# Optimization experiments

Measured on AMD Instinct MI355X. Metric: run time of the kernel, lower is better.

The kernel has to match this reference:

```python
import jax, jax.numpy as jnp
from jax import lax
import numpy as np

B, S, I = 128, 1024, 512
H = 512  # must equal I (W_hr/W_hi are applied to h)


def setup_inputs() -> dict:
    key = jax.random.key(0)
    ks = jax.random.split(key, 10)
    s = 1.0 / np.sqrt(H)
    return {
        "inputs": jax.random.normal(ks[0], (B, S, I), jnp.float32),
        "W_ih": jax.random.normal(ks[1], (I, H), jnp.float32) * s,
        "W_hh": jax.random.normal(ks[2], (H, H), jnp.float32) * s,
        "W_ir": jax.random.normal(ks[3], (I, 1), jnp.float32) * s,
        "W_hr": jax.random.normal(ks[4], (I, 1), jnp.float32) * s,
        "W_ii": jax.random.normal(ks[5], (I, 1), jnp.float32) * s,
        "W_hi": jax.random.normal(ks[6], (I, 1), jnp.float32) * s,
        "bias_h": jax.random.normal(ks[7], (H,), jnp.float32) * s,
        "bias_r": jax.random.normal(ks[8], (1,), jnp.float32) * s,
        "bias_i": jax.random.normal(ks[9], (1,), jnp.float32) * s,
    }


def reference(inputs, W_ih, W_hh, W_ir, W_hr, W_ii, W_hi, bias_h, bias_r, bias_i):
    b = inputs.shape[0]
    h_dim = W_hh.shape[0]
    # Precompute all input projections in one batched GEMM each.
    xh = inputs @ W_ih + bias_h            # (B,S,H)
    xr = inputs @ W_ir + bias_r            # (B,S,1)
    xi = inputs @ W_ii + bias_i            # (B,S,1)

    def step(h, xs):
        xh_t, xr_t, xi_t = xs              # (B,H), (B,1), (B,1)
        z = jax.nn.sigmoid(xr_t + h @ W_hr)        # update gate (B,1)
        r = jax.nn.sigmoid(xi_t + h @ W_hi)        # reset gate  (B,1)
        n = jnp.tanh(xh_t + (r * h) @ W_hh)        # candidate   (B,H)
        h_new = z * h + (1.0 - z) * n
        return h_new, h_new

    xs = (jnp.swapaxes(xh, 0, 1), jnp.swapaxes(xr, 0, 1), jnp.swapaxes(xi, 0, 1))
    h0 = jnp.zeros((b, h_dim), inputs.dtype)
    h_last, hs = lax.scan(step, h0, xs)    # hs: (S,B,H)
    return jnp.swapaxes(hs, 0, 1), h_last
```

## Files before the change

### kernel.cpp

```cpp
#include <hip/hip_runtime.h>
#include <hip/hip_bf16.h>

#define Bd 128
#define Sd 1024
#define Id 512
#define Hd 512

#define NG 8
#define NC 8
#define BB 16
#define JW 64

typedef __attribute__((ext_vector_type(8))) short short8;
typedef __attribute__((ext_vector_type(4))) float f32x4;

__device__ __forceinline__ unsigned int bf16_rn_bits(float x){
  unsigned int bx = __float_as_uint(x);
  return (bx + 0x7FFFu + ((bx >> 16) & 1u)) >> 16;
}

__global__ __launch_bounds__(256) void k_xh(const float* __restrict__ X,
                                            const float* __restrict__ W,
                                            const float* __restrict__ bias,
                                            float* __restrict__ out)
{
  const int bidm = blockIdx.x >> 2;
  const int bidn = blockIdx.x & 3;
  const int t  = threadIdx.x;
  const int tx = t & 15, ty = t >> 4;

  __shared__ __align__(16) float At[16][132];
  __shared__ __align__(16) float Bt[16][132];

  float acc[8][8];
  #pragma unroll
  for (int i = 0; i < 8; ++i)
    #pragma unroll
    for (int j = 0; j < 8; ++j) acc[i][j] = 0.f;

  const float* Xb = X + (size_t)bidm * 128 * Id;
  const float* Wb = W + bidn * 128;

  for (int k0 = 0; k0 < Id; k0 += 16) {
    #pragma unroll
    for (int f = t; f < 512; f += 256) {
      int m = f >> 2, c = (f & 3) * 4;
      float4 v = *(const float4*)(Xb + (size_t)m * Id + k0 + c);
      At[c + 0][m] = v.x; At[c + 1][m] = v.y; At[c + 2][m] = v.z; At[c + 3][m] = v.w;
    }
    #pragma unroll
    for (int f = t; f < 512; f += 256) {
      int kr = f >> 5, nc = (f & 31) * 4;
      *(float4*)&Bt[kr][nc] = *(const float4*)(Wb + (size_t)(k0 + kr) * Hd + nc);
    }
    __syncthreads();
    #pragma unroll
    for (int k = 0; k < 16; ++k) {
      float a[8], b[8];
      *(float4*)(a)     = *(float4*)&At[k][ty * 4];
      *(float4*)(a + 4) = *(float4*)&At[k][64 + ty * 4];
      *(float4*)(b)     = *(float4*)&Bt[k][tx * 4];
      *(float4*)(b + 4) = *(float4*)&Bt[k][64 + tx * 4];
      #pragma unroll
      for (int i = 0; i < 8; ++i)
        #pragma unroll
        for (int j = 0; j < 8; ++j)
          acc[i][j] = fmaf(a[i], b[j], acc[i][j]);
    }
    __syncthreads();
  }

  float bj[8];
  *(float4*)(bj)     = *(const float4*)(bias + bidn * 128 + tx * 4);
  *(float4*)(bj + 4) = *(const float4*)(bias + bidn * 128 + 64 + tx * 4);
  size_t obase = (size_t)bidm * 128 * Hd + bidn * 128;
  #pragma unroll
  for (int i = 0; i < 8; ++i) {
    int m = (i < 4) ? (ty * 4 + i) : (64 + ty * 4 + i - 4);
    float o[8];
    #pragma unroll
    for (int j = 0; j < 8; ++j) o[j] = acc[i][j] + bj[j];
    *(float4*)(out + obase + (size_t)m * Hd + tx * 4)      = *(float4*)(o);
    *(float4*)(out + obase + (size_t)m * Hd + 64 + tx * 4) = *(float4*)(o + 4);
  }
}

__global__ __launch_bounds__(256) void k_xri(const float* __restrict__ X,
                                             const float* __restrict__ Wir,
                                             const float* __restrict__ Wii,
                                             const float* __restrict__ br,
                                             const float* __restrict__ bi,
                                             float* __restrict__ xrp,
                                             float* __restrict__ xip)
{
  const int lane = threadIdx.x & 63;
  const int wv   = threadIdx.x >> 6;
  const size_t row = (size_t)blockIdx.x * 4 + wv;
  const float* xp = X + row * Id + lane * 8;
  float4 x0 = *(const float4*)(xp);
  float4 x1 = *(const float4*)(xp + 4);
  float4 r0 = *(const float4*)(Wir + lane * 8);
  float4 r1 = *(const float4*)(Wir + lane * 8 + 4);
  float4 i0 = *(const float4*)(Wii + lane * 8);
  float4 i1 = *(const float4*)(Wii + lane * 8 + 4);
  float sr = x0.x*r0.x + x0.y*r0.y + x0.z*r0.z + x0.w*r0.w
           + x1.x*r1.x + x1.y*r1.y + x1.z*r1.z + x1.w*r1.w;
  float si = x0.x*i0.x + x0.y*i0.y + x0.z*i0.z + x0.w*i0.w
           + x1.x*i1.x + x1.y*i1.y + x1.z*i1.z + x1.w*i1.w;
  #pragma unroll
  for (int o = 32; o; o >>= 1) { sr += __shfl_xor(sr, o, 64); si += __shfl_xor(si, o, 64); }
  if (lane == 0) { xrp[row] = sr + br[0]; xip[row] = si + bi[0]; }
}

__global__ __launch_bounds__(256, 1) void k_scan(
    const float* __restrict__ xr, const float* __restrict__ xi,
    const float* __restrict__ Whh, const float* __restrict__ Whr,
    const float* __restrict__ Whi,
    float* __restrict__ hs, float* __restrict__ hlast,
    float* __restrict__ xbuf, int* __restrict__ flags)
{
  const int bid  = blockIdx.x;
  const int g    = bid & 7;
  const int c    = bid >> 3;
  const int tid  = threadIdx.x;
  const int lane = tid & 63;
  const int wv   = tid >> 6;
  const int bBase = g * BB;
  const int jBase = c * JW;

  __shared__ __align__(16) float hsm[BB][Hd];
  __shared__ __align__(16) unsigned short hhi[BB * Hd];
  __shared__ __align__(16) unsigned short hlo[BB * Hd];
  __shared__ __align__(16) float whr_s[Hd];
  __shared__ __align__(16) float whi_s[Hd];
  __shared__ float zbuf[BB], rbuf[BB];

  for (int i = tid; i < Hd; i += 256) { whr_s[i] = Whr[i]; whi_s[i] = Whi[i]; }
  for (int i = tid; i < BB * Hd / 4; i += 256) ((float4*)hsm)[i] = make_float4(0, 0, 0, 0);
  for (int i = tid; i < BB * Hd / 2; i += 256) { ((unsigned int*)hhi)[i] = 0u; ((unsigned int*)hlo)[i] = 0u; }

  const int n16 = lane & 15, kq = lane >> 4;
  const int jglob = jBase + wv * 16 + n16;
  short8 wfh[16], wfl[16];
  #pragma unroll
  for (int kt = 0; kt < 16; ++kt) {
    short8 ph, pl;
    #pragma unroll
    for (int i = 0; i < 8; ++i) {
      int k = kt * 32 + kq * 8 + i;
      float x = Whh[(size_t)k * Hd + jglob];
      unsigned int hb = bf16_rn_bits(x);
      float hf = __uint_as_float(hb << 16);
      unsigned int lb = bf16_rn_bits(x - hf);
      ph[i] = (short)hb;
      pl[i] = (short)lb;
    }
    wfh[kt] = ph; wfl[kt] = pl;
  }
  __syncthreads();

  const int myflag = g * NC + c;

  for (int t = 0; t < Sd; ++t) {
    {
      int b = tid >> 4, l16 = tid & 15;
      float sr = 0.f, si = 0.f;
      #pragma unroll
      for (int kk = 0; kk < 8; ++kk) {
        float4 hv  = *(float4*)&hsm[b][kk * 64 + l16 * 4];
        float4 wr  = *(float4*)&whr_s[kk * 64 + l16 * 4];
        float4 wi2 = *(float4*)&whi_s[kk * 64 + l16 * 4];
        sr += hv.x*wr.x  + hv.y*wr.y  + hv.z*wr.z  + hv.w*wr.w;
        si += hv.x*wi2.x + hv.y*wi2.y + hv.z*wi2.z + hv.w*wi2.w;
      }
      #pragma unroll
      for (int o = 8; o; o >>= 1) { sr += __shfl_xor(sr, o, 64); si += __shfl_xor(si, o, 64); }
      if (l16 == 0) {
        size_t bg = bBase + b;
        zbuf[b] = 1.f / (1.f + __expf(-(xr[bg * Sd + t] + sr)));
        rbuf[b] = 1.f / (1.f + __expf(-(xi[bg * Sd + t] + si)));
      }
    }
    __syncthreads();

    float xhv[4];
    #pragma unroll
    for (int r2 = 0; r2 < 4; ++r2) {
      int m = (lane >> 4) * 4 + r2;
      xhv[r2] = hs[((size_t)(bBase + m) * Sd + t) * Hd + jglob];
    }

    f32x4 a0 = {0,0,0,0}, a1 = {0,0,0,0}, a2 = {0,0,0,0};
    {
      const int abase = (lane & 15) * 1024 + (lane >> 4) * 16;
      const int sw = (lane & 7) << 4;
      #pragma unroll
      for (int kt = 0; kt < 16; ++kt) {
        int off = (abase + kt * 64) ^ sw;
        short8 ah = *(short8*)((char*)hhi + off);
        short8 al = *(short8*)((char*)hlo + off);
        a0 = __builtin_amdgcn_mfma_f32_16x16x32_bf16(ah, wfh[kt], a0, 0, 0, 0);
        a1 = __builtin_amdgcn_mfma_f32_16x16x32_bf16(ah, wfl[kt], a1, 0, 0, 0);
        a2 = __builtin_amdgcn_mfma_f32_16x16x32_bf16(al, wfh[kt], a2, 0, 0, 0);
      }
    }

    {
      int par = (t + 1) & 1;
      float* xslot = xbuf + ((size_t)g * 2 + par) * BB * Hd;
      #pragma unroll
      for (int r2 = 0; r2 < 4; ++r2) {
        int m = (lane >> 4) * 4 + r2;
        float v  = a0[r2] + a1[r2] + a2[r2];
        float rr = rbuf[m], zz = zbuf[m];
        float xv = xhv[r2] + rr * v;
        float n  = 1.f - 2.f / (__expf(2.f * xv) + 1.f);
        float hnew = zz * hsm[m][jglob] + (1.f - zz) * n;
        hs[((size_t)(bBase + m) * Sd + t) * Hd + jglob] = hnew;
        if (t == Sd - 1) hlast[(size_t)(bBase + m) * Hd + jglob] = hnew;
        xslot[(size_t)m * Hd + jglob] = hnew;
      }
    }
    __syncthreads();
    if (tid == 0) {
      __threadfence();
      __hip_atomic_store(&flags[myflag], t + 1, __ATOMIC_RELAXED, __HIP_MEMORY_SCOPE_AGENT);
    }
    if (tid < NC) {
      while (__hip_atomic_load(&flags[g * NC + tid], __ATOMIC_RELAXED, __HIP_MEMORY_SCOPE_AGENT) <= t)
        __builtin_amdgcn_s_sleep(1);
    }
    __syncthreads();
    __threadfence();

    {
      int par = (t + 1) & 1;
      const float* xslot = xbuf + ((size_t)g * 2 + par) * BB * Hd;
      #pragma unroll
      for (int i = 0; i < 8; ++i) {
        int fid = i * 256 + tid;
        float4 hv = *(const float4*)(xslot + (size_t)fid * 4);
        int b = fid >> 7, kc = fid & 127;
        *(float4*)&hsm[b][kc * 4] = hv;
        float hf4[4] = {hv.x, hv.y, hv.z, hv.w};
        unsigned long long ph = 0ull, pl = 0ull;
        #pragma unroll
        for (int j2 = 0; j2 < 4; ++j2) {
          unsigned int hb = bf16_rn_bits(hf4[j2]);
          float hff = __uint_as_float(hb << 16);
          unsigned int lb = bf16_rn_bits(hf4[j2] - hff);
          ph |= (unsigned long long)(hb & 0xFFFFu) << (16 * j2);
          pl |= (unsigned long long)(lb & 0xFFFFu) << (16 * j2);
        }
        int off = (b * 1024 + kc * 8) ^ ((b & 7) << 4);
        *(unsigned long long*)((char*)hhi + off) = ph;
        *(unsigned long long*)((char*)hlo + off) = pl;
      }
    }
    __syncthreads();
  }
}

extern "C" void kernel_launch(void* const* d_in, const int* in_sizes, int n_in,
                              void* d_out, int out_size, void* d_ws, size_t ws_size,
                              hipStream_t stream)
{
  const float* X    = (const float*)d_in[0];
  const float* Wih  = (const float*)d_in[1];
  const float* Whh  = (const float*)d_in[2];
  const float* Wir  = (const float*)d_in[3];
  const float* Whr  = (const float*)d_in[4];
  const float* Wii  = (const float*)d_in[5];
  const float* Whi  = (const float*)d_in[6];
  const float* bh   = (const float*)d_in[7];
  const float* br   = (const float*)d_in[8];
  const float* bi   = (const float*)d_in[9];
  (void)in_sizes; (void)n_in; (void)out_size;

  float* out   = (float*)d_out;
  float* hlast = out + (size_t)Bd * Sd * Hd;

  char*  ws    = (char*)d_ws;
  float* xr    = (float*)(ws);
  float* xi    = (float*)(ws + (size_t)Bd * Sd * 4);
  float* xbuf  = (float*)(ws + (size_t)Bd * Sd * 8);
  int*   flags = (int*)  (ws + (size_t)Bd * Sd * 8 + (size_t)NG * 2 * BB * Hd * 4);
  (void)ws_size;

  hipMemsetAsync(flags, 0, NG * NC * sizeof(int), stream);
  k_xh  <<<dim3(4096),            dim3(256), 0, stream>>>(X, Wih, bh, out);
  k_xri <<<dim3(Bd * Sd / 4),     dim3(256), 0, stream>>>(X, Wir, Wii, br, bi, xr, xi);
  k_scan<<<dim3(NG * NC),         dim3(256), 0, stream>>>(xr, xi, Whh, Whr, Whi, out, hlast, xbuf, flags);
}
```

Before: 10.70 ms.

## Use one 1024-thread block per batch group and MFMA split-bf16 for input GEMM

The scan kernel drops the 64-block grid and its global flag-based inter-block barrier. It uses 8 blocks of 1024 threads, each holding all of W_hh in registers as split bf16 fragments, so every timestep synchronises only inside a block. The input-projection GEMM moves from fp32 FMA to bf16 hi/lo split MFMA, and the next step's xh/xr/xi values are prefetched. The trade-off is that only 8 CUs run the serial recurrence, with heavy register pressure per thread (64 short8 weight fragments), against removing the cross-block global-memory handshake on every step.

```diff
diff --git a/kernel.cpp b/kernel.cpp
--- a/kernel.cpp
+++ b/kernel.cpp
@@ -7,9 +7,7 @@
 #define Hd 512
 
 #define NG 8
-#define NC 8
 #define BB 16
-#define JW 64
 
 typedef __attribute__((ext_vector_type(8))) short short8;
 typedef __attribute__((ext_vector_type(4))) float f32x4;
@@ -17,6 +15,12 @@
 __device__ __forceinline__ unsigned int bf16_rn_bits(float x){
   unsigned int bx = __float_as_uint(x);
   return (bx + 0x7FFFu + ((bx >> 16) & 1u)) >> 16;
+}
+__device__ __forceinline__ void bf16_split(float x, unsigned short& hi, unsigned short& lo){
+  unsigned int hb = bf16_rn_bits(x);
+  float hf = __uint_as_float(hb << 16);
+  hi = (unsigned short)hb;
+  lo = (unsigned short)bf16_rn_bits(x - hf);
 }
 
 __global__ __launch_bounds__(256) void k_xh(const float* __restrict__ X,
@@ -26,63 +30,98 @@
 {
   const int bidm = blockIdx.x >> 2;
   const int bidn = blockIdx.x & 3;
-  const int t  = threadIdx.x;
-  const int tx = t & 15, ty = t >> 4;
-
-  __shared__ __align__(16) float At[16][132];
-  __shared__ __align__(16) float Bt[16][132];
-
-  float acc[8][8];
-  #pragma unroll
-  for (int i = 0; i < 8; ++i)
-    #pragma unroll
-    for (int j = 0; j < 8; ++j) acc[i][j] = 0.f;
+  const int tid  = threadIdx.x;
+  const int lane = tid & 63;
+  const int wv   = tid >> 6;
+  const int wr   = wv >> 1, wc = wv & 1;
+  const int n16  = lane & 15, kq = lane >> 4;
+
+  __shared__ __align__(16) unsigned short Ah[128 * 64];
+  __shared__ __align__(16) unsigned short Al[128 * 64];
+  __shared__ __align__(16) unsigned short Bh[128 * 64];
+  __shared__ __align__(16) unsigned short Bl[128 * 64];
+
+  f32x4 acc[4][4];
+  #pragma unroll
+  for (int i = 0; i < 4; ++i)
+    #pragma unroll
+    for (int j = 0; j < 4; ++j) acc[i][j] = (f32x4){0.f, 0.f, 0.f, 0.f};
 
   const float* Xb = X + (size_t)bidm * 128 * Id;
   const float* Wb = W + bidn * 128;
 
-  for (int k0 = 0; k0 < Id; k0 += 16) {
-    #pragma unroll
-    for (int f = t; f < 512; f += 256) {
-      int m = f >> 2, c = (f & 3) * 4;
-      float4 v = *(const float4*)(Xb + (size_t)m * Id + k0 + c);
-      At[c + 0][m] = v.x; At[c + 1][m] = v.y; At[c + 2][m] = v.z; At[c + 3][m] = v.w;
-    }
-    #pragma unroll
-    for (int f = t; f < 512; f += 256) {
-      int kr = f >> 5, nc = (f & 31) * 4;
-      *(float4*)&Bt[kr][nc] = *(const float4*)(Wb + (size_t)(k0 + kr) * Hd + nc);
-    }
-    __syncthreads();
-    #pragma unroll
-    for (int k = 0; k < 16; ++k) {
-      float a[8], b[8];
-      *(float4*)(a)     = *(float4*)&At[k][ty * 4];
-      *(float4*)(a + 4) = *(float4*)&At[k][64 + ty * 4];
-      *(float4*)(b)     = *(float4*)&Bt[k][tx * 4];
-      *(float4*)(b + 4) = *(float4*)&Bt[k][64 + tx * 4];
-      #pragma unroll
-      for (int i = 0; i < 8; ++i)
+  for (int k0 = 0; k0 < Id; k0 += 64) {
+    #pragma unroll
+    for (int f = 0; f < 8; ++f) {
+      int idx = f * 256 + tid;
+      int m = idx >> 4, kc = (idx & 15) * 4;
+      float4 v = *(const float4*)(Xb + (size_t)m * Id + k0 + kc);
+      unsigned short h0,l0,h1,l1,h2,l2,h3,l3;
+      bf16_split(v.x,h0,l0); bf16_split(v.y,h1,l1);
+      bf16_split(v.z,h2,l2); bf16_split(v.w,h3,l3);
+      unsigned long long ph = (unsigned long long)h0 | ((unsigned long long)h1<<16)
+                            | ((unsigned long long)h2<<32) | ((unsigned long long)h3<<48);
+      unsigned long long pl = (unsigned long long)l0 | ((unsigned long long)l1<<16)
+                            | ((unsigned long long)l2<<32) | ((unsigned long long)l3<<48);
+      int off = (m * 128 + kc * 2) ^ ((m & 7) << 4);
+      *(unsigned long long*)((char*)Ah + off) = ph;
+      *(unsigned long long*)((char*)Al + off) = pl;
+    }
+    #pragma unroll
+    for (int f = 0; f < 8; ++f) {
+      int idx = f * 256 + tid;
+      int kr = idx >> 5, nc = (idx & 31) * 4;
+      float4 v = *(const float4*)(Wb + (size_t)(k0 + kr) * Hd + nc);
+      float vv[4] = {v.x, v.y, v.z, v.w};
+      #pragma unroll
+      for (int q = 0; q < 4; ++q) {
+        unsigned short h, l; bf16_split(vv[q], h, l);
+        int n = nc + q;
+        int off = (n * 128 + kr * 2) ^ ((n & 7) << 4);
+        *(unsigned short*)((char*)Bh + off) = h;
+        *(unsigned short*)((char*)Bl + off) = l;
+      }
+    }
+    __syncthreads();
+    #pragma unroll
+    for (int kt = 0; kt < 2; ++kt) {
+      short8 amh[4], aml[4];
+      #pragma unroll
+      for (int mt = 0; mt < 4; ++mt) {
+        int m = wr * 64 + mt * 16 + n16;
+        int off = (m * 128 + kt * 64 + kq * 16) ^ ((m & 7) << 4);
+        amh[mt] = *(short8*)((char*)Ah + off);
+        aml[mt] = *(short8*)((char*)Al + off);
+      }
+      #pragma unroll
+      for (int ntl = 0; ntl < 4; ++ntl) {
+        int n = wc * 64 + ntl * 16 + n16;
+        int off = (n * 128 + kt * 64 + kq * 16) ^ ((n & 7) << 4);
+        short8 bh = *(short8*)((char*)Bh + off);
+        short8 bl = *(short8*)((char*)Bl + off);
         #pragma unroll
-        for (int j = 0; j < 8; ++j)
-          acc[i][j] = fmaf(a[i], b[j], acc[i][j]);
+        for (int mt = 0; mt < 4; ++mt) {
+          acc[mt][ntl] = __builtin_amdgcn_mfma_f32_16x16x32_bf16(amh[mt], bh, acc[mt][ntl], 0,0,0);
+          acc[mt][ntl] = __builtin_amdgcn_mfma_f32_16x16x32_bf16(amh[mt], bl, acc[mt][ntl], 0,0,0);
+          acc[mt][ntl] = __builtin_amdgcn_mfma_f32_16x16x32_bf16(aml[mt], bh, acc[mt][ntl], 0,0,0);
+        }
+      }
     }
     __syncthreads();
   }
-
-  float bj[8];
-  *(float4*)(bj)     = *(const float4*)(bias + bidn * 128 + tx * 4);
-  *(float4*)(bj + 4) = *(const float4*)(bias + bidn * 128 + 64 + tx * 4);
-  size_t obase = (size_t)bidm * 128 * Hd + bidn * 128;
-  #pragma unroll
-  for (int i = 0; i < 8; ++i) {
-    int m = (i < 4) ? (ty * 4 + i) : (64 + ty * 4 + i - 4);
-    float o[8];
-    #pragma unroll
-    for (int j = 0; j < 8; ++j) o[j] = acc[i][j] + bj[j];
-    *(float4*)(out + obase + (size_t)m * Hd + tx * 4)      = *(float4*)(o);
-    *(float4*)(out + obase + (size_t)m * Hd + 64 + tx * 4) = *(float4*)(o + 4);
-  }
+  float bj[4];
+  #pragma unroll
+  for (int ntl = 0; ntl < 4; ++ntl) bj[ntl] = bias[bidn * 128 + wc * 64 + ntl * 16 + n16];
+  #pragma unroll
+  for (int mt = 0; mt < 4; ++mt)
+    #pragma unroll
+    for (int ntl = 0; ntl < 4; ++ntl)
+      #pragma unroll
+      for (int r = 0; r < 4; ++r) {
+        size_t m = (size_t)bidm * 128 + wr * 64 + mt * 16 + kq * 4 + r;
+        int n = bidn * 128 + wc * 64 + ntl * 16 + n16;
+        out[m * Hd + n] = acc[mt][ntl][r] + bj[ntl];
+      }
 }
 
 __global__ __launch_bounds__(256) void k_xri(const float* __restrict__ X,
@@ -112,21 +151,18 @@
   if (lane == 0) { xrp[row] = sr + br[0]; xip[row] = si + bi[0]; }
 }
 
-__global__ __launch_bounds__(256, 1) void k_scan(
+__global__ __launch_bounds__(1024) void k_scan(
     const float* __restrict__ xr, const float* __restrict__ xi,
     const float* __restrict__ Whh, const float* __restrict__ Whr,
     const float* __restrict__ Whi,
-    float* __restrict__ hs, float* __restrict__ hlast,
-    float* __restrict__ xbuf, int* __restrict__ flags)
+    float* __restrict__ hs, float* __restrict__ hlast)
 {
-  const int bid  = blockIdx.x;
-  const int g    = bid & 7;
-  const int c    = bid >> 3;
+  const int g    = blockIdx.x;
   const int tid  = threadIdx.x;
   const int lane = tid & 63;
-  const int wv   = tid >> 6;
+  const int w    = tid >> 6;
+  const int n16  = lane & 15, kq = lane >> 4;
   const int bBase = g * BB;
-  const int jBase = c * JW;
 
   __shared__ __align__(16) float hsm[BB][Hd];
   __shared__ __align__(16) unsigned short hhi[BB * Hd];
@@ -135,129 +171,128 @@
   __shared__ __align__(16) float whi_s[Hd];
   __shared__ float zbuf[BB], rbuf[BB];
 
-  for (int i = tid; i < Hd; i += 256) { whr_s[i] = Whr[i]; whi_s[i] = Whi[i]; }
-  for (int i = tid; i < BB * Hd / 4; i += 256) ((float4*)hsm)[i] = make_float4(0, 0, 0, 0);
-  for (int i = tid; i < BB * Hd / 2; i += 256) { ((unsigned int*)hhi)[i] = 0u; ((unsigned int*)hlo)[i] = 0u; }
-
-  const int n16 = lane & 15, kq = lane >> 4;
-  const int jglob = jBase + wv * 16 + n16;
-  short8 wfh[16], wfl[16];
-  #pragma unroll
-  for (int kt = 0; kt < 16; ++kt) {
-    short8 ph, pl;
-    #pragma unroll
-    for (int i = 0; i < 8; ++i) {
-      int k = kt * 32 + kq * 8 + i;
-      float x = Whh[(size_t)k * Hd + jglob];
-      unsigned int hb = bf16_rn_bits(x);
-      float hf = __uint_as_float(hb << 16);
-      unsigned int lb = bf16_rn_bits(x - hf);
-      ph[i] = (short)hb;
-      pl[i] = (short)lb;
-    }
-    wfh[kt] = ph; wfl[kt] = pl;
+  if (tid < Hd) { whr_s[tid] = Whr[tid]; whi_s[tid] = Whi[tid]; }
+  for (int i = tid; i < BB * Hd / 4; i += 1024) ((float4*)hsm)[i] = make_float4(0,0,0,0);
+  for (int i = tid; i < BB * Hd / 2; i += 1024) { ((unsigned int*)hhi)[i] = 0u; ((unsigned int*)hlo)[i] = 0u; }
+
+  short8 wfh0[16], wfl0[16], wfh1[16], wfl1[16];
+  {
+    const float* wp = Whh + (size_t)(w * 32 + n16);
+    #pragma unroll
+    for (int kt = 0; kt < 16; ++kt) {
+      short8 ph0, pl0, ph1, pl1;
+      #pragma unroll
+      for (int i = 0; i < 8; ++i) {
+        size_t k = (size_t)(kt * 32 + kq * 8 + i);
+        unsigned short h, l;
+        bf16_split(wp[k * Hd], h, l);        ph0[i] = (short)h; pl0[i] = (short)l;
+        bf16_split(wp[k * Hd + 16], h, l);   ph1[i] = (short)h; pl1[i] = (short)l;
+      }
+      wfh0[kt] = ph0; wfl0[kt] = pl0; wfh1[kt] = ph1; wfl1[kt] = pl1;
+    }
   }
   __syncthreads();
 
-  const int myflag = g * NC + c;
+  float xh_cur[2][4], xh_nxt[2][4];
+  #pragma unroll
+  for (int nt = 0; nt < 2; ++nt)
+    #pragma unroll
+    for (int r = 0; r < 4; ++r)
+      xh_cur[nt][r] = hs[((size_t)(bBase + kq * 4 + r) * Sd + 0) * Hd + w * 32 + nt * 16 + n16];
+  float xrc = 0.f, xic = 0.f;
+  if (lane == 0) { xrc = xr[(size_t)(bBase + w) * Sd]; xic = xi[(size_t)(bBase + w) * Sd]; }
 
   for (int t = 0; t < Sd; ++t) {
     {
-      int b = tid >> 4, l16 = tid & 15;
       float sr = 0.f, si = 0.f;
       #pragma unroll
-      for (int kk = 0; kk < 8; ++kk) {
-        float4 hv  = *(float4*)&hsm[b][kk * 64 + l16 * 4];
-        float4 wr  = *(float4*)&whr_s[kk * 64 + l16 * 4];
-        float4 wi2 = *(float4*)&whi_s[kk * 64 + l16 * 4];
-        sr += hv.x*wr.x  + hv.y*wr.y  + hv.z*wr.z  + hv.w*wr.w;
-        si += hv.x*wi2.x + hv.y*wi2.y + hv.z*wi2.z + hv.w*wi2.w;
-      }
-      #pragma unroll
-      for (int o = 8; o; o >>= 1) { sr += __shfl_xor(sr, o, 64); si += __shfl_xor(si, o, 64); }
-      if (l16 == 0) {
-        size_t bg = bBase + b;
-        zbuf[b] = 1.f / (1.f + __expf(-(xr[bg * Sd + t] + sr)));
-        rbuf[b] = 1.f / (1.f + __expf(-(xi[bg * Sd + t] + si)));
-      }
-    }
-    __syncthreads();
-
-    float xhv[4];
-    #pragma unroll
-    for (int r2 = 0; r2 < 4; ++r2) {
-      int m = (lane >> 4) * 4 + r2;
-      xhv[r2] = hs[((size_t)(bBase + m) * Sd + t) * Hd + jglob];
-    }
-
-    f32x4 a0 = {0,0,0,0}, a1 = {0,0,0,0}, a2 = {0,0,0,0};
+      for (int u = 0; u < 2; ++u) {
+        float4 hv = *(float4*)&hsm[w][lane * 8 + u * 4];
+        float4 wr4 = *(float4*)&whr_s[lane * 8 + u * 4];
+        float4 wi4 = *(float4*)&whi_s[lane * 8 + u * 4];
+        sr += hv.x*wr4.x + hv.y*wr4.y + hv.z*wr4.z + hv.w*wr4.w;
+        si += hv.x*wi4.x + hv.y*wi4.y + hv.z*wi4.z + hv.w*wi4.w;
+      }
+      #pragma unroll
+      for (int o = 32; o; o >>= 1) { sr += __shfl_xor(sr, o, 64); si += __shfl_xor(si, o, 64); }
+      if (lane == 0) {
+        zbuf[w] = 1.f / (1.f + __expf(-(xrc + sr)));
+        rbuf[w] = 1.f / (1.f + __expf(-(xic + si)));
+      }
+    }
+    __syncthreads();
+
+    const int tt = (t + 1 < Sd) ? (t + 1) : t;
+    float xrn = 0.f, xin = 0.f;
+    if (lane == 0) {
+      xrn = xr[(size_t)(bBase + w) * Sd + tt];
+      xin = xi[(size_t)(bBase + w) * Sd + tt];
+    }
+    #pragma unroll
+    for (int nt = 0; nt < 2; ++nt)
+      #pragma unroll
+      for (int r = 0; r < 4; ++r)
+        xh_nxt[nt][r] = hs[((size_t)(bBase + kq * 4 + r) * Sd + tt) * Hd + w * 32 + nt * 16 + n16];
+
+    f32x4 a00={0,0,0,0}, a01={0,0,0,0}, a02={0,0,0,0};
+    f32x4 a10={0,0,0,0}, a11={0,0,0,0}, a12={0,0,0,0};
     {
-      const int abase = (lane & 15) * 1024 + (lane >> 4) * 16;
-      const int sw = (lane & 7) << 4;
+      const int abase = (lane & 15) * 1024 + kq * 16;
+      const int sw = ((lane & 15) & 7) << 4;
       #pragma unroll
       for (int kt = 0; kt < 16; ++kt) {
         int off = (abase + kt * 64) ^ sw;
         short8 ah = *(short8*)((char*)hhi + off);
         short8 al = *(short8*)((char*)hlo + off);
-        a0 = __builtin_amdgcn_mfma_f32_16x16x32_bf16(ah, wfh[kt], a0, 0, 0, 0);
-        a1 = __builtin_amdgcn_mfma_f32_16x16x32_bf16(ah, wfl[kt], a1, 0, 0, 0);
-        a2 = __builtin_amdgcn_mfma_f32_16x16x32_bf16(al, wfh[kt], a2, 0, 0, 0);
-      }
-    }
-
-    {
-      int par = (t + 1) & 1;
-      float* xslot = xbuf + ((size_t)g * 2 + par) * BB * Hd;
-      #pragma unroll
-      for (int r2 = 0; r2 < 4; ++r2) {
-        int m = (lane >> 4) * 4 + r2;
-        float v  = a0[r2] + a1[r2] + a2[r2];
-        float rr = rbuf[m], zz = zbuf[m];
-        float xv = xhv[r2] + rr * v;
-        float n  = 1.f - 2.f / (__expf(2.f * xv) + 1.f);
-        float hnew = zz * hsm[m][jglob] + (1.f - zz) * n;
-        hs[((size_t)(bBase + m) * Sd + t) * Hd + jglob] = hnew;
-        if (t == Sd - 1) hlast[(size_t)(bBase + m) * Hd + jglob] = hnew;
-        xslot[(size_t)m * Hd + jglob] = hnew;
-      }
-    }
-    __syncthreads();
-    if (tid == 0) {
-      __threadfence();
-      __hip_atomic_store(&flags[myflag], t + 1, __ATOMIC_RELAXED, __HIP_MEMORY_SCOPE_AGENT);
-    }
-    if (tid < NC) {
-      while (__hip_atomic_load(&flags[g * NC + tid], __ATOMIC_RELAXED, __HIP_MEMORY_SCOPE_AGENT) <= t)
-        __builtin_amdgcn_s_sleep(1);
-    }
-    __syncthreads();
-    __threadfence();
-
-    {
-      int par = (t + 1) & 1;
-      const float* xslot = xbuf + ((size_t)g * 2 + par) * BB * Hd;
-      #pragma unroll
-      for (int i = 0; i < 8; ++i) {
-        int fid = i * 256 + tid;
-        float4 hv = *(const float4*)(xslot + (size_t)fid * 4);
-        int b = fid >> 7, kc = fid & 127;
-        *(float4*)&hsm[b][kc * 4] = hv;
-        float hf4[4] = {hv.x, hv.y, hv.z, hv.w};
-        unsigned long long ph = 0ull, pl = 0ull;
-        #pragma unroll
-        for (int j2 = 0; j2 < 4; ++j2) {
-          unsigned int hb = bf16_rn_bits(hf4[j2]);
-          float hff = __uint_as_float(hb << 16);
-          unsigned int lb = bf16_rn_bits(hf4[j2] - hff);
-          ph |= (unsigned long long)(hb & 0xFFFFu) << (16 * j2);
-          pl |= (unsigned long long)(lb & 0xFFFFu) << (16 * j2);
-        }
-        int off = (b * 1024 + kc * 8) ^ ((b & 7) << 4);
-        *(unsigned long long*)((char*)hhi + off) = ph;
-        *(unsigned long long*)((char*)hlo + off) = pl;
-      }
-    }
-    __syncthreads();
+        a00 = __builtin_amdgcn_mfma_f32_16x16x32_bf16(ah, wfh0[kt], a00, 0,0,0);
+        a01 = __builtin_amdgcn_mfma_f32_16x16x32_bf16(ah, wfl0[kt], a01, 0,0,0);
+        a02 = __builtin_amdgcn_mfma_f32_16x16x32_bf16(al, wfh0[kt], a02, 0,0,0);
+        a10 = __builtin_amdgcn_mfma_f32_16x16x32_bf16(ah, wfh1[kt], a10, 0,0,0);
+        a11 = __builtin_amdgcn_mfma_f32_16x16x32_bf16(ah, wfl1[kt], a11, 0,0,0);
+        a12 = __builtin_amdgcn_mfma_f32_16x16x32_bf16(al, wfh1[kt], a12, 0,0,0);
+      }
+    }
+
+    float hn[2][4];
+    #pragma unroll
+    for (int nt = 0; nt < 2; ++nt) {
+      f32x4 v4 = nt ? (a10 + a11 + a12) : (a00 + a01 + a02);
+      int j = w * 32 + nt * 16 + n16;
+      #pragma unroll
+      for (int r = 0; r < 4; ++r) {
+        int row = kq * 4 + r;
+        float rr = rbuf[row], zz = zbuf[row];
+        float xv = xh_cur[nt][r] + rr * v4[r];
+        float nn = 1.f - 2.f / (__expf(2.f * xv) + 1.f);
+        float hnew = zz * hsm[row][j] + (1.f - zz) * nn;
+        hs[((size_t)(bBase + row) * Sd + t) * Hd + j] = hnew;
+        if (t == Sd - 1) hlast[(size_t)(bBase + row) * Hd + j] = hnew;
+        hn[nt][r] = hnew;
+      }
+    }
+    __syncthreads();
+
+    #pragma unroll
+    for (int nt = 0; nt < 2; ++nt) {
+      int j = w * 32 + nt * 16 + n16;
+      #pragma unroll
+      for (int r = 0; r < 4; ++r) {
+        int row = kq * 4 + r;
+        float hnew = hn[nt][r];
+        hsm[row][j] = hnew;
+        unsigned short hb, lb; bf16_split(hnew, hb, lb);
+        int off = (row * 1024 + j * 2) ^ ((row & 7) << 4);
+        *(unsigned short*)((char*)hhi + off) = hb;
+        *(unsigned short*)((char*)hlo + off) = lb;
+      }
+    }
+    __syncthreads();
+
+    #pragma unroll
+    for (int nt = 0; nt < 2; ++nt)
+      #pragma unroll
+      for (int r = 0; r < 4; ++r) xh_cur[nt][r] = xh_nxt[nt][r];
+    xrc = xrn; xic = xin;
   }
 }
 
@@ -275,20 +310,16 @@
   const float* bh   = (const float*)d_in[7];
   const float* br   = (const float*)d_in[8];
   const float* bi   = (const float*)d_in[9];
-  (void)in_sizes; (void)n_in; (void)out_size;
+  (void)in_sizes; (void)n_in; (void)out_size; (void)ws_size;
 
   float* out   = (float*)d_out;
   float* hlast = out + (size_t)Bd * Sd * Hd;
 
-  char*  ws    = (char*)d_ws;
-  float* xr    = (float*)(ws);
-  float* xi    = (float*)(ws + (size_t)Bd * Sd * 4);
-  float* xbuf  = (float*)(ws + (size_t)Bd * Sd * 8);
-  int*   flags = (int*)  (ws + (size_t)Bd * Sd * 8 + (size_t)NG * 2 * BB * Hd * 4);
-  (void)ws_size;
-
-  hipMemsetAsync(flags, 0, NG * NC * sizeof(int), stream);
-  k_xh  <<<dim3(4096),            dim3(256), 0, stream>>>(X, Wih, bh, out);
-  k_xri <<<dim3(Bd * Sd / 4),     dim3(256), 0, stream>>>(X, Wir, Wii, br, bi, xr, xi);
-  k_scan<<<dim3(NG * NC),         dim3(256), 0, stream>>>(xr, xi, Whh, Whr, Whi, out, hlast, xbuf, flags);
-}
+  char*  ws = (char*)d_ws;
+  float* xr = (float*)(ws);
+  float* xi = (float*)(ws + (size_t)Bd * Sd * 4);
+
+  k_xh  <<<dim3(4096),        dim3(256),  0, stream>>>(X, Wih, bh, out);
+  k_xri <<<dim3(Bd * Sd / 4), dim3(256),  0, stream>>>(X, Wir, Wii, br, bi, xr, xi);
+  k_scan<<<dim3(NG),          dim3(1024), 0, stream>>>(xr, xi, Whh, Whr, Whi, out, hlast);
+}
```

Result: slower. 31.34 ms (+192.8%).
